# Kernel optimization log

Measured on AMD Instinct MI355X. Metric: run time of the kernel, lower is better.

## Reference

```python
import jax, jax.numpy as jnp
import numpy as np

HIDDEN = 1024
HEADS = 16
HEAD_DIM = HIDDEN // HEADS


def setup_inputs() -> dict:
    key = jax.random.key(0)
    ks = jax.random.split(key, 9)
    B, S = 2, 2048
    std = 1.0 / np.sqrt(HIDDEN)
    inp = {
        'hidden_states': jax.random.normal(ks[0], (B, S, HIDDEN), dtype=jnp.float32),
        'attention_mask': jnp.ones((B, S), dtype=jnp.int32),
        'wq': jax.random.normal(ks[1], (HIDDEN, HIDDEN), dtype=jnp.float32) * std,
        'bq': jnp.zeros((HIDDEN,), dtype=jnp.float32),
        'wk': jax.random.normal(ks[2], (HIDDEN, HIDDEN), dtype=jnp.float32) * std,
        'bk': jnp.zeros((HIDDEN,), dtype=jnp.float32),
        'wv': jax.random.normal(ks[3], (HIDDEN, HIDDEN), dtype=jnp.float32) * std,
        'bv': jnp.zeros((HIDDEN,), dtype=jnp.float32),
        'wo': jax.random.normal(ks[4], (HIDDEN, HIDDEN), dtype=jnp.float32) * std,
        'bo': jnp.zeros((HIDDEN,), dtype=jnp.float32),
    }
    return inp


def reference(hidden_states, attention_mask, wq, bq, wk, bk, wv, bv, wo, bo):
    B, S, H = hidden_states.shape
    def heads(x):  # [B,S,H] -> [B,nh,S,hd]
        return x.reshape(B, S, HEADS, HEAD_DIM).transpose(0, 2, 1, 3)
    q = heads(hidden_states @ wq + bq)
    k = heads(hidden_states @ wk + bk)
    v = heads(hidden_states @ wv + bv)
    scores = jnp.einsum('bhqd,bhkd->bhqk', q, k) / np.sqrt(HEAD_DIM).astype(np.float32)
    causal = jnp.tril(jnp.ones((S, S), dtype=bool))  # True = keep
    keep = causal[None, None] & (attention_mask[:, None, None, :] != 0)
    scores = jnp.where(keep, scores, -jnp.inf)
    probs = jax.nn.softmax(scores, axis=-1)
    out = jnp.einsum('bhqk,bhkd->bhqd', probs, v)  # [B,nh,S,hd]
    out = out.transpose(0, 2, 1, 3).reshape(B, S, H)
    return out @ wo + bo
```

## Files before the change

### kernel.cpp

```cpp
#include <hip/hip_runtime.h>

#define HID   1024
#define SLEN  2048
#define NHEAD 16
#define HDIM  64
#define SC2L  0.18033688f
#define KPAD  72
#define VPAD  68

typedef unsigned short u16;
typedef _Float16 f16;
using bf16x8 = __attribute__((ext_vector_type(8))) short;
using f16x4  = __attribute__((ext_vector_type(4))) f16;
using f32x4  = __attribute__((ext_vector_type(4))) float;

typedef __attribute__((address_space(1))) void gvoid;
typedef __attribute__((address_space(3))) void lvoid;

__device__ __forceinline__ u16 f2bf(float f) {
  union { float f; unsigned u; } v; v.f = f;
  unsigned u = v.u;
  return (u16)((u + 0x7fffu + ((u >> 16) & 1u)) >> 16);
}
__device__ __forceinline__ u16 bf2h(u16 b) {
  union { unsigned u; float f; } v; v.u = ((unsigned)b) << 16;
  union { f16 h; u16 u; } c; c.h = (f16)v.f;
  return c.u;
}

__device__ __forceinline__ void async_ld16(const u16* g, u16* l) {
  __builtin_amdgcn_global_load_lds((gvoid*)g, (lvoid*)l, 16, 0, 0);
}

__global__ __launch_bounds__(256) void prep_kernel(const float* __restrict__ x,
                                                   const float* __restrict__ wq,
                                                   const float* __restrict__ wk,
                                                   const float* __restrict__ wv,
                                                   const float* __restrict__ wo,
                                                   u16* __restrict__ xb,
                                                   u16* __restrict__ wt) {
  const int tid = threadIdx.x;
  if (blockIdx.z == 4) {
    const int bid = blockIdx.y * 32 + blockIdx.x;
#pragma unroll
    for (int it = 0; it < 4; ++it) {
      const int i = bid * 1024 + it * 256 + tid;
      float4 v = ((const float4*)x)[i];
      ushort4 o;
      o.x = f2bf(v.x); o.y = f2bf(v.y); o.z = f2bf(v.z); o.w = f2bf(v.w);
      ((ushort4*)xb)[i] = o;
    }
    return;
  }
  const float* src = (blockIdx.z == 0) ? wq : (blockIdx.z == 1) ? wk
                   : (blockIdx.z == 2) ? wv : wo;
  u16* dst = wt + (size_t)blockIdx.z * (HID * HID);
  __shared__ float tile[32][33];
  const int n0 = blockIdx.x * 32, k0 = blockIdx.y * 32;
  const int xx = tid & 31, yy = tid >> 5;
  for (int i = yy; i < 32; i += 8)
    tile[i][xx] = src[(size_t)(k0 + i) * HID + n0 + xx];
  __syncthreads();
  for (int i = yy; i < 32; i += 8)
    dst[(size_t)(n0 + i) * HID + k0 + xx] = f2bf(tile[xx][i]);
}

__global__ __launch_bounds__(256) void gemm_qkv_kernel(const u16* __restrict__ A,
                                                       const u16* __restrict__ Bt,
                                                       const float* __restrict__ bq,
                                                       const float* __restrict__ bk,
                                                       const float* __restrict__ bv,
                                                       u16* __restrict__ Qb,
                                                       u16* __restrict__ Kb,
                                                       u16* __restrict__ Vb) {
  __shared__ u16 sA[128 * 32];
  __shared__ u16 sB[128 * 32];
  const int tid  = threadIdx.x;
  const int wave = tid >> 6, lane = tid & 63;
  const int quad = lane >> 4, l16 = lane & 15;
  const int n0g = blockIdx.x * 128;
  const int region = blockIdx.x >> 3;
  const int colbase = (blockIdx.x & 7) * 128;
  const int m0 = blockIdx.y * 128;
  const int wm = (wave & 1) * 64, wn = (wave >> 1) * 64;

  f32x4 acc[4][4] = {};
  const int srow = lane >> 2;
  const int scol = (lane & 3) * 8;

  for (int kt = 0; kt < HID; kt += 32) {
    __syncthreads();
    for (int c = wave; c < 8; c += 4) {
      async_ld16(A  + (size_t)(m0  + c * 16 + srow) * HID + kt + scol, &sA[c * 512]);
      async_ld16(Bt + (size_t)(n0g + c * 16 + srow) * HID + kt + scol, &sB[c * 512]);
    }
    __syncthreads();

    bf16x8 af[4], bfr[4];
#pragma unroll
    for (int t = 0; t < 4; ++t) {
      af[t]  = *(const bf16x8*)&sA[(wm + t * 16 + l16) * 32 + quad * 8];
      bfr[t] = *(const bf16x8*)&sB[(wn + t * 16 + l16) * 32 + quad * 8];
    }
#pragma unroll
    for (int mt = 0; mt < 4; ++mt)
#pragma unroll
      for (int nt = 0; nt < 4; ++nt)
        acc[mt][nt] = __builtin_amdgcn_mfma_f32_16x16x32_bf16(af[mt], bfr[nt],
                                                              acc[mt][nt], 0, 0, 0);
  }

  const float* bias = (region == 0) ? bq : (region == 1) ? bk : bv;
  u16* C = (region == 0) ? Qb : (region == 1) ? Kb : Vb;
  float bvv[4];
#pragma unroll
  for (int nt = 0; nt < 4; ++nt) bvv[nt] = bias[colbase + wn + nt * 16 + l16];
#pragma unroll
  for (int mt = 0; mt < 4; ++mt)
#pragma unroll
    for (int r = 0; r < 4; ++r) {
      const int row = m0 + wm + mt * 16 + quad * 4 + r;
#pragma unroll
      for (int nt = 0; nt < 4; ++nt) {
        const int col = colbase + wn + nt * 16 + l16;
        C[(size_t)row * HID + col] = f2bf(acc[mt][nt][r] + bvv[nt]);
      }
    }
}

__global__ __launch_bounds__(256) void gemm_o_kernel(const u16* __restrict__ A,
                                                     const u16* __restrict__ Bt,
                                                     const float* __restrict__ bias,
                                                     float* __restrict__ Cf) {
  __shared__ u16 sA[64 * 32];
  __shared__ u16 sB[128 * 32];
  const int tid  = threadIdx.x;
  const int wave = tid >> 6, lane = tid & 63;
  const int quad = lane >> 4, l16 = lane & 15;
  const int n0 = blockIdx.x * 128;
  const int m0 = blockIdx.y * 64;
  const int wn = wave * 32;

  f32x4 acc[4][2] = {};
  const int srow = lane >> 2;
  const int scol = (lane & 3) * 8;

  for (int kt = 0; kt < HID; kt += 32) {
    __syncthreads();
    for (int c = wave; c < 12; c += 4) {
      if (c < 4) async_ld16(A  + (size_t)(m0 + c * 16 + srow) * HID + kt + scol, &sA[c * 512]);
      else       async_ld16(Bt + (size_t)(n0 + (c - 4) * 16 + srow) * HID + kt + scol,
                            &sB[(c - 4) * 512]);
    }
    __syncthreads();

    bf16x8 af[4], bfr[2];
#pragma unroll
    for (int t = 0; t < 4; ++t)
      af[t] = *(const bf16x8*)&sA[(t * 16 + l16) * 32 + quad * 8];
#pragma unroll
    for (int t = 0; t < 2; ++t)
      bfr[t] = *(const bf16x8*)&sB[(wn + t * 16 + l16) * 32 + quad * 8];
#pragma unroll
    for (int mt = 0; mt < 4; ++mt)
#pragma unroll
      for (int nt = 0; nt < 2; ++nt)
        acc[mt][nt] = __builtin_amdgcn_mfma_f32_16x16x32_bf16(af[mt], bfr[nt],
                                                              acc[mt][nt], 0, 0, 0);
  }

  float bvv[2];
#pragma unroll
  for (int nt = 0; nt < 2; ++nt) bvv[nt] = bias[n0 + wn + nt * 16 + l16];
#pragma unroll
  for (int mt = 0; mt < 4; ++mt)
#pragma unroll
    for (int r = 0; r < 4; ++r) {
      const int row = m0 + mt * 16 + quad * 4 + r;
#pragma unroll
      for (int nt = 0; nt < 2; ++nt)
        Cf[(size_t)row * HID + n0 + wn + nt * 16 + l16] = acc[mt][nt][r] + bvv[nt];
    }
}

__global__ __launch_bounds__(256, 2) void flash_attn_kernel(const u16* __restrict__ Q,
                                                            const u16* __restrict__ K,
                                                            const u16* __restrict__ V,
                                                            const int* __restrict__ mask,
                                                            u16* __restrict__ O) {
  const int xb = blockIdx.x, h = blockIdx.y, b = blockIdx.z;
  const int tid  = threadIdx.x;
  const int wave = tid >> 6, lane = tid & 63;
  const int quad = lane >> 4, l16 = lane & 15;

  __shared__ u16 Ks[2][64 * KPAD];
  __shared__ u16 Vt[2][64 * VPAD];
  __shared__ float maskadd[2][64];
  __shared__ float lbuf[4][64];
  float* Obuf0 = (float*)&Ks[0][0];
  float* Obuf1 = (float*)&Vt[0][0];

  const u16* Kh = K + (size_t)b * SLEN * HID + h * HDIM;
  const u16* Vh = V + (size_t)b * SLEN * HID + h * HDIM;

  const int srow = tid >> 2;
  const int sc8  = (tid & 3) * 8;

  for (int phase = 0; phase < 2; ++phase) {
    const int qt = phase ? (31 - xb) : xb;
    const int q0 = qt * 64;

    bf16x8 qb[4][2];
#pragma unroll
    for (int nt = 0; nt < 4; ++nt) {
      const u16* qp = Q + (size_t)(b * SLEN + q0 + nt * 16 + l16) * HID + h * HDIM + quad * 8;
      qb[nt][0] = *(const bf16x8*)qp;
      qb[nt][1] = *(const bf16x8*)(qp + 32);
    }

    f32x4 oacc[4][4] = {};
    float l_part[4] = {0.f, 0.f, 0.f, 0.f};

    bf16x8 kr0, kr1, vr0, vr1;
    int mreg = 0;
    {
      const u16* kg = Kh + (size_t)srow * HID + sc8;
      kr0 = *(const bf16x8*)kg;  kr1 = *(const bf16x8*)(kg + 32);
      const u16* vg = Vh + (size_t)srow * HID + sc8;
      vr0 = *(const bf16x8*)vg;  vr1 = *(const bf16x8*)(vg + 32);
      if (tid < 64) mreg = mask[b * SLEN + tid];
    }

    for (int j = 0; j <= qt; ++j) {
      const int buf = j & 1;
      *(bf16x8*)&Ks[buf][srow * KPAD + sc8]      = kr0;
      *(bf16x8*)&Ks[buf][srow * KPAD + sc8 + 32] = kr1;
      {
        const u16* v0 = (const u16*)&vr0;
        const u16* v1 = (const u16*)&vr1;
#pragma unroll
        for (int e = 0; e < 8; ++e) {
          Vt[buf][(sc8 + e) * VPAD + srow]      = bf2h(v0[e]);
          Vt[buf][(sc8 + e + 32) * VPAD + srow] = bf2h(v1[e]);
        }
      }
      if (tid < 64) maskadd[buf][tid] = mreg ? 0.f : -1e30f;
      __syncthreads();

      if (j < qt) {
        const u16* kg = Kh + (size_t)((j + 1) * 64 + srow) * HID + sc8;
        kr0 = *(const bf16x8*)kg;  kr1 = *(const bf16x8*)(kg + 32);
        const u16* vg = Vh + (size_t)((j + 1) * 64 + srow) * HID + sc8;
        vr0 = *(const bf16x8*)vg;  vr1 = *(const bf16x8*)(vg + 32);
        if (tid < 64) mreg = mask[b * SLEN + (j + 1) * 64 + tid];
      }

      const bf16x8 ka0 = *(const bf16x8*)&Ks[buf][(wave * 16 + l16) * KPAD + quad * 8];
      const bf16x8 ka1 = *(const bf16x8*)&Ks[buf][(wave * 16 + l16) * KPAD + quad * 8 + 32];
      const float4 ma  = *(const float4*)&maskadd[buf][wave * 16 + quad * 4];
      const float* map = (const float*)&ma;

      float p[4][4];
#pragma unroll
      for (int nt = 0; nt < 4; ++nt) {
        f32x4 z = {0.f, 0.f, 0.f, 0.f};
        z = __builtin_amdgcn_mfma_f32_16x16x32_bf16(ka0, qb[nt][0], z, 0, 0, 0);
        z = __builtin_amdgcn_mfma_f32_16x16x32_bf16(ka1, qb[nt][1], z, 0, 0, 0);
#pragma unroll
        for (int r = 0; r < 4; ++r)
          p[nt][r] = exp2f(fmaf(z[r], SC2L, map[r]));
      }
      if (j == qt) {
#pragma unroll
        for (int nt = 0; nt < 4; ++nt)
#pragma unroll
          for (int r = 0; r < 4; ++r)
            if (wave * 16 + quad * 4 + r > nt * 16 + l16) p[nt][r] = 0.f;
      }

      f16x4 pb[4];
#pragma unroll
      for (int nt = 0; nt < 4; ++nt) {
        l_part[nt] += (p[nt][0] + p[nt][1]) + (p[nt][2] + p[nt][3]);
        pb[nt][0] = (f16)p[nt][0]; pb[nt][1] = (f16)p[nt][1];
        pb[nt][2] = (f16)p[nt][2]; pb[nt][3] = (f16)p[nt][3];
      }

#pragma unroll
      for (int dt = 0; dt < 4; ++dt) {
        const f16x4 va = *(const f16x4*)&Vt[buf][(dt * 16 + l16) * VPAD + wave * 16 + quad * 4];
#pragma unroll
        for (int nt = 0; nt < 4; ++nt)
          oacc[dt][nt] = __builtin_amdgcn_mfma_f32_16x16x16f16(va, pb[nt], oacc[dt][nt], 0, 0, 0);
      }
    }

#pragma unroll
    for (int nt = 0; nt < 4; ++nt) {
      l_part[nt] += __shfl_xor(l_part[nt], 16);
      l_part[nt] += __shfl_xor(l_part[nt], 32);
    }
    __syncthreads();

    if (quad == 0)
#pragma unroll
      for (int nt = 0; nt < 4; ++nt) lbuf[wave][nt * 16 + l16] = l_part[nt];

    if ((wave & 1) == 0) {
      float* ob = (wave == 0) ? Obuf0 : Obuf1;
#pragma unroll
      for (int dt = 0; dt < 4; ++dt)
#pragma unroll
        for (int nt = 0; nt < 4; ++nt)
#pragma unroll
          for (int r = 0; r < 4; ++r)
            ob[(dt * 16 + quad * 4 + r) * 65 + nt * 16 + l16] = oacc[dt][nt][r];
    }
    __syncthreads();
    if (wave & 1) {
      float* ob = (wave == 1) ? Obuf0 : Obuf1;
#pragma unroll
      for (int dt = 0; dt < 4; ++dt)
#pragma unroll
        for (int nt = 0; nt < 4; ++nt)
#pragma unroll
          for (int r = 0; r < 4; ++r)
            ob[(dt * 16 + quad * 4 + r) * 65 + nt * 16 + l16] += oacc[dt][nt][r];
    }
    __syncthreads();

    {
      const int q  = tid >> 2;
      const int dc = tid & 3;
      const float l = lbuf[0][q] + lbuf[1][q] + lbuf[2][q] + lbuf[3][q];
      const float inv = 1.f / l;
      u16 ob[16];
#pragma unroll
      for (int e = 0; e < 16; ++e) {
        const int d = dc * 16 + e;
        ob[e] = f2bf((Obuf0[d * 65 + q] + Obuf1[d * 65 + q]) * inv);
      }
      u16* op = O + (size_t)(b * SLEN + q0 + q) * HID + h * HDIM + dc * 16;
      *(bf16x8*)op       = *(bf16x8*)&ob[0];
      *(bf16x8*)(op + 8) = *(bf16x8*)&ob[8];
    }
    __syncthreads();
  }
}

extern "C" void kernel_launch(void* const* d_in, const int* in_sizes, int n_in,
                              void* d_out, int out_size, void* d_ws, size_t ws_size,
                              hipStream_t stream) {
  const float* x    = (const float*)d_in[0];
  const int*   mask = (const int*)d_in[1];
  const float* wq   = (const float*)d_in[2];
  const float* bq   = (const float*)d_in[3];
  const float* wk   = (const float*)d_in[4];
  const float* bk   = (const float*)d_in[5];
  const float* wv   = (const float*)d_in[6];
  const float* bv   = (const float*)d_in[7];
  const float* wo   = (const float*)d_in[8];
  const float* bo   = (const float*)d_in[9];
  float* out = (float*)d_out;

  char* ws = (char*)d_ws;
  u16* XBF = (u16*)(ws);
  u16* WT  = (u16*)(ws + (8u  << 20));
  u16* QBF = (u16*)(ws + (16u << 20));
  u16* KBF = (u16*)(ws + (24u << 20));
  u16* VBF = (u16*)(ws + (32u << 20));
  u16* ATT = (u16*)(ws);

  prep_kernel<<<dim3(32, 32, 5), 256, 0, stream>>>(x, wq, wk, wv, wo, XBF, WT);
  gemm_qkv_kernel<<<dim3(24, 32), 256, 0, stream>>>(XBF, WT, bq, bk, bv, QBF, KBF, VBF);
  flash_attn_kernel<<<dim3(16, NHEAD, 2), 256, 0, stream>>>(QBF, KBF, VBF, mask, ATT);
  gemm_o_kernel<<<dim3(8, 64), 256, 0, stream>>>(ATT, WT + (3u << 20), bo, out);
}
```

Baseline: 207.8 us.

## Emit V pre-transposed in fp16 from QKV GEMM and async-load tiles in attention

```diff
diff --git a/kernel.cpp b/kernel.cpp
--- a/kernel.cpp
+++ b/kernel.cpp
@@ -5,8 +5,6 @@
 #define NHEAD 16
 #define HDIM  64
 #define SC2L  0.18033688f
-#define KPAD  72
-#define VPAD  68
 
 typedef unsigned short u16;
 typedef _Float16 f16;
@@ -21,11 +19,6 @@
   union { float f; unsigned u; } v; v.f = f;
   unsigned u = v.u;
   return (u16)((u + 0x7fffu + ((u >> 16) & 1u)) >> 16);
-}
-__device__ __forceinline__ u16 bf2h(u16 b) {
-  union { unsigned u; float f; } v; v.u = ((unsigned)b) << 16;
-  union { f16 h; u16 u; } c; c.h = (f16)v.f;
-  return c.u;
 }
 
 __device__ __forceinline__ void async_ld16(const u16* g, u16* l) {
@@ -72,9 +65,10 @@
                                                        const float* __restrict__ bv,
                                                        u16* __restrict__ Qb,
                                                        u16* __restrict__ Kb,
-                                                       u16* __restrict__ Vb) {
-  __shared__ u16 sA[128 * 32];
-  __shared__ u16 sB[128 * 32];
+                                                       u16* __restrict__ VTf) {
+  __shared__ u16 smem[8192];
+  u16* sA = smem;
+  u16* sB = smem + 4096;
   const int tid  = threadIdx.x;
   const int wave = tid >> 6, lane = tid & 63;
   const int quad = lane >> 4, l16 = lane & 15;
@@ -111,10 +105,46 @@
   }
 
   const float* bias = (region == 0) ? bq : (region == 1) ? bk : bv;
-  u16* C = (region == 0) ? Qb : (region == 1) ? Kb : Vb;
   float bvv[4];
 #pragma unroll
   for (int nt = 0; nt < 4; ++nt) bvv[nt] = bias[colbase + wn + nt * 16 + l16];
+
+  if (region == 2) {
+    const int bb = m0 >> 11;
+    const int m0loc = m0 & 2047;
+    const int h0 = colbase >> 6;
+    u16* T = smem;
+#pragma unroll
+    for (int h2 = 0; h2 < 2; ++h2) {
+      __syncthreads();
+      if ((wave >> 1) == h2) {
+#pragma unroll
+        for (int mt = 0; mt < 4; ++mt)
+#pragma unroll
+          for (int nt = 0; nt < 4; ++nt)
+#pragma unroll
+            for (int r = 0; r < 4; ++r) {
+              const int sl = (wave & 1) * 64 + mt * 16 + quad * 4 + r;
+              const int dl = nt * 16 + l16;
+              union { f16 h; u16 u; } cv;
+              cv.h = (f16)(acc[mt][nt][r] + bvv[nt]);
+              T[dl * 128 + (((sl >> 3) ^ l16) * 8) + (sl & 7)] = cv.u;
+            }
+      }
+      __syncthreads();
+      const int d = tid >> 2, sg = (tid & 3) * 4;
+      u16* drow = VTf + (size_t)((bb * NHEAD + h0 + h2) * HDIM + d) * SLEN + m0loc;
+#pragma unroll
+      for (int cc = 0; cc < 4; ++cc) {
+        const int cl = sg + cc;
+        const int ph = cl ^ (d & 15);
+        *(bf16x8*)(drow + cl * 8) = *(const bf16x8*)&T[d * 128 + ph * 8];
+      }
+    }
+    return;
+  }
+
+  u16* C = (region == 0) ? Qb : Kb;
 #pragma unroll
   for (int mt = 0; mt < 4; ++mt)
 #pragma unroll
@@ -185,7 +215,7 @@
 
 __global__ __launch_bounds__(256, 2) void flash_attn_kernel(const u16* __restrict__ Q,
                                                             const u16* __restrict__ K,
-                                                            const u16* __restrict__ V,
+                                                            const u16* __restrict__ VT,
                                                             const int* __restrict__ mask,
                                                             u16* __restrict__ O) {
   const int xb = blockIdx.x, h = blockIdx.y, b = blockIdx.z;
@@ -193,18 +223,19 @@
   const int wave = tid >> 6, lane = tid & 63;
   const int quad = lane >> 4, l16 = lane & 15;
 
-  __shared__ u16 Ks[2][64 * KPAD];
-  __shared__ u16 Vt[2][64 * VPAD];
-  __shared__ float maskadd[2][64];
-  __shared__ float lbuf[4][64];
-  float* Obuf0 = (float*)&Ks[0][0];
-  float* Obuf1 = (float*)&Vt[0][0];
-
-  const u16* Kh = K + (size_t)b * SLEN * HID + h * HDIM;
-  const u16* Vh = V + (size_t)b * SLEN * HID + h * HDIM;
-
-  const int srow = tid >> 2;
-  const int sc8  = (tid & 3) * 8;
+  __shared__ alignas(16) char smraw[35840];
+  u16*   Ks  = (u16*)smraw;
+  u16*   Vt  = (u16*)(smraw + 16384);
+  float* Ob0 = (float*)smraw;
+  float* Ob1 = (float*)(smraw + 16896);
+  float* lb  = (float*)(smraw + 33792);
+
+  const u16* Kh  = K  + (size_t)b * SLEN * HID + h * HDIM;
+  const u16* Vth = VT + (size_t)((b * NHEAD + h) * HDIM) * SLEN;
+
+  const int srow8 = lane >> 3;
+  const int gch   = (lane & 7) ^ srow8;
+  const int rx    = l16 & 7;
 
   for (int phase = 0; phase < 2; ++phase) {
     const int qt = phase ? (31 - xb) : xb;
@@ -221,44 +252,39 @@
     f32x4 oacc[4][4] = {};
     float l_part[4] = {0.f, 0.f, 0.f, 0.f};
 
-    bf16x8 kr0, kr1, vr0, vr1;
-    int mreg = 0;
     {
-      const u16* kg = Kh + (size_t)srow * HID + sc8;
-      kr0 = *(const bf16x8*)kg;  kr1 = *(const bf16x8*)(kg + 32);
-      const u16* vg = Vh + (size_t)srow * HID + sc8;
-      vr0 = *(const bf16x8*)vg;  vr1 = *(const bf16x8*)(vg + 32);
-      if (tid < 64) mreg = mask[b * SLEN + tid];
-    }
+      const int r0 = wave * 16 + srow8;
+      async_ld16(Kh  + (size_t)r0 * HID + gch * 8,        Ks + wave * 1024);
+      async_ld16(Kh  + (size_t)(r0 + 8) * HID + gch * 8,  Ks + wave * 1024 + 512);
+      async_ld16(Vth + (size_t)r0 * SLEN + gch * 8,       Vt + wave * 1024);
+      async_ld16(Vth + (size_t)(r0 + 8) * SLEN + gch * 8, Vt + wave * 1024 + 512);
+    }
+    __syncthreads();
 
     for (int j = 0; j <= qt; ++j) {
       const int buf = j & 1;
-      *(bf16x8*)&Ks[buf][srow * KPAD + sc8]      = kr0;
-      *(bf16x8*)&Ks[buf][srow * KPAD + sc8 + 32] = kr1;
-      {
-        const u16* v0 = (const u16*)&vr0;
-        const u16* v1 = (const u16*)&vr1;
-#pragma unroll
-        for (int e = 0; e < 8; ++e) {
-          Vt[buf][(sc8 + e) * VPAD + srow]      = bf2h(v0[e]);
-          Vt[buf][(sc8 + e + 32) * VPAD + srow] = bf2h(v1[e]);
-        }
-      }
-      if (tid < 64) maskadd[buf][tid] = mreg ? 0.f : -1e30f;
-      __syncthreads();
+      u16* KsB = Ks + buf * 4096;
+      u16* VtB = Vt + buf * 4096;
 
       if (j < qt) {
-        const u16* kg = Kh + (size_t)((j + 1) * 64 + srow) * HID + sc8;
-        kr0 = *(const bf16x8*)kg;  kr1 = *(const bf16x8*)(kg + 32);
-        const u16* vg = Vh + (size_t)((j + 1) * 64 + srow) * HID + sc8;
-        vr0 = *(const bf16x8*)vg;  vr1 = *(const bf16x8*)(vg + 32);
-        if (tid < 64) mreg = mask[b * SLEN + (j + 1) * 64 + tid];
-      }
-
-      const bf16x8 ka0 = *(const bf16x8*)&Ks[buf][(wave * 16 + l16) * KPAD + quad * 8];
-      const bf16x8 ka1 = *(const bf16x8*)&Ks[buf][(wave * 16 + l16) * KPAD + quad * 8 + 32];
-      const float4 ma  = *(const float4*)&maskadd[buf][wave * 16 + quad * 4];
-      const float* map = (const float*)&ma;
+        const int nb = (buf ^ 1) * 4096;
+        const int jn = (j + 1) * 64;
+        const int r0 = wave * 16 + srow8;
+        async_ld16(Kh  + (size_t)(jn + r0) * HID + gch * 8,       Ks + nb + wave * 1024);
+        async_ld16(Kh  + (size_t)(jn + r0 + 8) * HID + gch * 8,   Ks + nb + wave * 1024 + 512);
+        async_ld16(Vth + (size_t)r0 * SLEN + jn + gch * 8,        Vt + nb + wave * 1024);
+        async_ld16(Vth + (size_t)(r0 + 8) * SLEN + jn + gch * 8,  Vt + nb + wave * 1024 + 512);
+      }
+
+      const int4 mi = *(const int4*)(mask + b * SLEN + j * 64 + wave * 16 + quad * 4);
+      float map[4];
+      map[0] = mi.x ? 0.f : -1e30f;  map[1] = mi.y ? 0.f : -1e30f;
+      map[2] = mi.z ? 0.f : -1e30f;  map[3] = mi.w ? 0.f : -1e30f;
+
+      const u16* kp = KsB + (wave * 16 + l16) * 64;
+      const int ph0 = quad ^ rx;
+      const bf16x8 ka0 = *(const bf16x8*)(kp + ph0 * 8);
+      const bf16x8 ka1 = *(const bf16x8*)(kp + (ph0 ^ 4) * 8);
 
       float p[4][4];
 #pragma unroll
@@ -286,13 +312,16 @@
         pb[nt][2] = (f16)p[nt][2]; pb[nt][3] = (f16)p[nt][3];
       }
 
+      const int phv = (wave * 2 + (quad >> 1)) ^ rx;
+      const int vsub = phv * 8 + (quad & 1) * 4;
 #pragma unroll
       for (int dt = 0; dt < 4; ++dt) {
-        const f16x4 va = *(const f16x4*)&Vt[buf][(dt * 16 + l16) * VPAD + wave * 16 + quad * 4];
+        const f16x4 va = *(const f16x4*)(VtB + (dt * 16 + l16) * 64 + vsub);
 #pragma unroll
         for (int nt = 0; nt < 4; ++nt)
           oacc[dt][nt] = __builtin_amdgcn_mfma_f32_16x16x16f16(va, pb[nt], oacc[dt][nt], 0, 0, 0);
       }
+      __syncthreads();
     }
 
 #pragma unroll
@@ -300,45 +329,43 @@
       l_part[nt] += __shfl_xor(l_part[nt], 16);
       l_part[nt] += __shfl_xor(l_part[nt], 32);
     }
-    __syncthreads();
-
     if (quad == 0)
 #pragma unroll
-      for (int nt = 0; nt < 4; ++nt) lbuf[wave][nt * 16 + l16] = l_part[nt];
+      for (int nt = 0; nt < 4; ++nt) lb[wave * 64 + nt * 16 + l16] = l_part[nt];
 
     if ((wave & 1) == 0) {
-      float* ob = (wave == 0) ? Obuf0 : Obuf1;
+      float* ob = (wave == 0) ? Ob0 : Ob1;
 #pragma unroll
       for (int dt = 0; dt < 4; ++dt)
 #pragma unroll
         for (int nt = 0; nt < 4; ++nt)
 #pragma unroll
           for (int r = 0; r < 4; ++r)
-            ob[(dt * 16 + quad * 4 + r) * 65 + nt * 16 + l16] = oacc[dt][nt][r];
+            ob[(dt * 16 + quad * 4 + r) * 66 + nt * 16 + l16] = oacc[dt][nt][r];
     }
     __syncthreads();
     if (wave & 1) {
-      float* ob = (wave == 1) ? Obuf0 : Obuf1;
+      float* ob = (wave == 1) ? Ob0 : Ob1;
 #pragma unroll
       for (int dt = 0; dt < 4; ++dt)
 #pragma unroll
         for (int nt = 0; nt < 4; ++nt)
 #pragma unroll
           for (int r = 0; r < 4; ++r)
-            ob[(dt * 16 + quad * 4 + r) * 65 + nt * 16 + l16] += oacc[dt][nt][r];
+            ob[(dt * 16 + quad * 4 + r) * 66 + nt * 16 + l16] += oacc[dt][nt][r];
     }
     __syncthreads();
 
     {
       const int q  = tid >> 2;
       const int dc = tid & 3;
-      const float l = lbuf[0][q] + lbuf[1][q] + lbuf[2][q] + lbuf[3][q];
+      const float l = lb[q] + lb[64 + q] + lb[128 + q] + lb[192 + q];
       const float inv = 1.f / l;
       u16 ob[16];
 #pragma unroll
       for (int e = 0; e < 16; ++e) {
         const int d = dc * 16 + e;
-        ob[e] = f2bf((Obuf0[d * 65 + q] + Obuf1[d * 65 + q]) * inv);
+        ob[e] = f2bf((Ob0[d * 66 + q] + Ob1[d * 66 + q]) * inv);
       }
       u16* op = O + (size_t)(b * SLEN + q0 + q) * HID + h * HDIM + dc * 16;
       *(bf16x8*)op       = *(bf16x8*)&ob[0];
@@ -368,11 +395,11 @@
   u16* WT  = (u16*)(ws + (8u  << 20));
   u16* QBF = (u16*)(ws + (16u << 20));
   u16* KBF = (u16*)(ws + (24u << 20));
-  u16* VBF = (u16*)(ws + (32u << 20));
+  u16* VTF = (u16*)(ws + (32u << 20));
   u16* ATT = (u16*)(ws);
 
   prep_kernel<<<dim3(32, 32, 5), 256, 0, stream>>>(x, wq, wk, wv, wo, XBF, WT);
-  gemm_qkv_kernel<<<dim3(24, 32), 256, 0, stream>>>(XBF, WT, bq, bk, bv, QBF, KBF, VBF);
-  flash_attn_kernel<<<dim3(16, NHEAD, 2), 256, 0, stream>>>(QBF, KBF, VBF, mask, ATT);
+  gemm_qkv_kernel<<<dim3(24, 32), 256, 0, stream>>>(XBF, WT, bq, bk, bv, QBF, KBF, VTF);
+  flash_attn_kernel<<<dim3(16, NHEAD, 2), 256, 0, stream>>>(QBF, KBF, VTF, mask, ATT);
   gemm_o_kernel<<<dim3(8, 64), 256, 0, stream>>>(ATT, WT + (3u << 20), bo, out);
 }
```

New measurement: 205.2 us. No clear change (-1.2%).
